# Kernel tuning notes

Hardware: AMD Instinct MI355X
Metric: run time of the kernel (lower is better)

The kernel has to match this reference:

```python
import jax, jax.numpy as jnp
import numpy as np

B, T = 512, 8192
DT = jnp.float32(1e-3)


def setup_inputs() -> dict:
    key = jax.random.key(0)
    k1, k2, k3, k4 = jax.random.split(key, 4)
    # scale noise so the 8192-step linear recurrence stays well-conditioned
    xicovs = jax.random.normal(k1, (B, T, 2, 2), jnp.float32) * 0.05
    dy = jax.random.normal(k2, (B, T, 2), jnp.float32) * 0.05
    coeffs_A = jax.random.uniform(k3, (2, 2), jnp.float32, -0.05, 0.05)  # 'uniform' init kernel
    C = jax.random.normal(k4, (2, 2), jnp.float32)
    return {"xicovs": xicovs, "dy": dy, "coeffs_A": coeffs_A, "C": C}


def reference(xicovs, dy, coeffs_A, C):
    # xicovs: [B,T,2,2], dy: [B,T,2]
    Bv = xicovs.shape[0]
    # initial state [1,0] broadcast over batch
    x0 = jnp.broadcast_to(jnp.array([1.0, 0.0], jnp.float32), (Bv, 2))
    xi_t = jnp.swapaxes(xicovs, 0, 1)  # [T,B,2,2]
    dy_t = jnp.swapaxes(dy, 0, 1)      # [T,B,2]

    def step(x, inp):
        xic, dyt = inp  # [B,2,2], [B,2]
        # cell emits C @ x_prev * dt
        out = jnp.einsum('ij,bj->bi', C, x) * DT
        A_minus_xiC = coeffs_A - jnp.einsum('bij,jk->bik', xic, C)  # [B,2,2]
        dx = jnp.einsum('bij,bj->bi', A_minus_xiC, x) * DT + jnp.einsum('bij,bj->bi', xic, dyt)
        return x + dx, out

    _, outs = jax.lax.scan(step, x0, (xi_t, dy_t))  # outs: [T,B,2]
    return jnp.swapaxes(outs, 0, 1)  # [B,T,2] (return_sequences=True)
```

## Files before the change

### kernel.cpp

```cpp
#include <hip/hip_runtime.h>


#define B_   512
#define T_   8192
#define LPT  8
#define NT   1024
static_assert(NT * LPT == T_, "one block covers one batch");

struct Aff { float m00, m01, m10, m11, v0, v1; };

__device__ __forceinline__ Aff aff_compose(const Aff& L, const Aff& E) {
    Aff r;
    r.m00 = L.m00*E.m00 + L.m01*E.m10;
    r.m01 = L.m00*E.m01 + L.m01*E.m11;
    r.m10 = L.m10*E.m00 + L.m11*E.m10;
    r.m11 = L.m10*E.m01 + L.m11*E.m11;
    r.v0  = L.m00*E.v0  + L.m01*E.v1 + L.v0;
    r.v1  = L.m10*E.v0  + L.m11*E.v1 + L.v1;
    return r;
}

__device__ __forceinline__ Aff aff_identity() {
    Aff r; r.m00 = 1.f; r.m01 = 0.f; r.m10 = 0.f; r.m11 = 1.f; r.v0 = 0.f; r.v1 = 0.f;
    return r;
}

__global__ __launch_bounds__(NT, 4) void grm_fused(
    const float* __restrict__ xic, const float* __restrict__ dy,
    const float* __restrict__ Aptr, const float* __restrict__ Cptr,
    float4* __restrict__ out4)
{
    __shared__ float4 lds4[16 * 256];

    const int b    = blockIdx.x;
    const int tid  = threadIdx.x;
    const int lane = tid & 63;
    const int wave = tid >> 6;

    float4* slice = lds4 + wave * 256;

    const float DT = 1e-3f;
    const float cd00 = Cptr[0]*DT, cd01 = Cptr[1]*DT;
    const float cd10 = Cptr[2]*DT, cd11 = Cptr[3]*DT;
    const float i00 = 1.0f + Aptr[0]*DT, i01 = Aptr[1]*DT;
    const float i10 = Aptr[2]*DT,        i11 = 1.0f + Aptr[3]*DT;

    const int wbase = b * T_ + wave * 512;
    const float4* xw = (const float4*)xic + wbase;
    const float4* dw = (const float4*)dy  + (wbase >> 1);
    float4*       ow = out4 + (wbase >> 1);

    float4 t[8], u[4];
    #pragma unroll
    for (int j = 0; j < 8; ++j) t[j] = xw[j*64 + lane];
    #pragma unroll
    for (int j = 0; j < 4; ++j) u[j] = dw[j*64 + lane];

    float4 a[LPT];
    #pragma unroll
    for (int rr = 0; rr < 2; ++rr) {
        #pragma unroll
        for (int jj = 0; jj < 4; ++jj) {
            int j = 4*rr + jj;
            int f = j*64 + lane;
            int rel = (f >> 3) & 31;
            slice[rel*8 + ((lane & 7) ^ (rel & 7))] = t[j];
        }
        if ((lane >> 5) == rr) {
            int rel = lane & 31;
            #pragma unroll
            for (int s = 0; s < LPT; ++s)
                a[s] = slice[rel*8 + (s ^ (rel & 7))];
        }
    }

    #pragma unroll
    for (int j = 0; j < 4; ++j) {
        int f = j*64 + lane;
        int o = f >> 2;
        slice[o*4 + ((lane & 3) ^ (o & 3))] = u[j];
    }
    float4 d[4];
    #pragma unroll
    for (int s = 0; s < 4; ++s)
        d[s] = slice[lane*4 + (s ^ (lane & 3))];

#define STEP_MAP(i, S)                                                  \
    {                                                                   \
        const float4 x4 = a[i];                                         \
        const float dyx = ((i)&1) ? d[(i)>>1].z : d[(i)>>1].x;          \
        const float dyy = ((i)&1) ? d[(i)>>1].w : d[(i)>>1].y;          \
        (S).m00 = i00 - (x4.x*cd00 + x4.y*cd10);                        \
        (S).m01 = i01 - (x4.x*cd01 + x4.y*cd11);                        \
        (S).m10 = i10 - (x4.z*cd00 + x4.w*cd10);                        \
        (S).m11 = i11 - (x4.z*cd01 + x4.w*cd11);                        \
        (S).v0  = x4.x*dyx + x4.y*dyy;                                  \
        (S).v1  = x4.z*dyx + x4.w*dyy;                                  \
    }

    Aff P;
    STEP_MAP(0, P);
    #pragma unroll
    for (int i = 1; i < LPT; ++i) { Aff s; STEP_MAP(i, s); P = aff_compose(s, P); }

    Aff S = P;
    #pragma unroll
    for (int sh = 1; sh < 64; sh <<= 1) {
        Aff q;
        q.m00 = __shfl_up(S.m00, sh); q.m01 = __shfl_up(S.m01, sh);
        q.m10 = __shfl_up(S.m10, sh); q.m11 = __shfl_up(S.m11, sh);
        q.v0  = __shfl_up(S.v0,  sh); q.v1  = __shfl_up(S.v1,  sh);
        if (lane >= sh) S = aff_compose(S, q);
    }

    if (lane == 63) {
        float* h = (float*)slice;
        h[0] = S.m00; h[1] = S.m01; h[2] = S.m10; h[3] = S.m11;
        h[4] = S.v0;  h[5] = S.v1;
    }
    __syncthreads();

    Aff Ew = aff_identity();
    for (int w = 0; w < wave; ++w) {
        const float* h = (const float*)(lds4 + w * 256);
        Aff t2;
        t2.m00 = h[0]; t2.m01 = h[1]; t2.m10 = h[2]; t2.m11 = h[3];
        t2.v0  = h[4]; t2.v1  = h[5];
        Ew = aff_compose(t2, Ew);
    }
    __syncthreads();

    Aff El;
    El.m00 = __shfl_up(S.m00, 1); El.m01 = __shfl_up(S.m01, 1);
    El.m10 = __shfl_up(S.m10, 1); El.m11 = __shfl_up(S.m11, 1);
    El.v0  = __shfl_up(S.v0,  1); El.v1  = __shfl_up(S.v1,  1);
    if (lane == 0) El = aff_identity();

    Aff E = aff_compose(El, Ew);
    float x0 = E.m00 + E.v0;
    float x1 = E.m10 + E.v1;

    float4 o4[4];
    #pragma unroll
    for (int i = 0; i < LPT; ++i) {
        float oxx = cd00*x0 + cd01*x1;
        float oyy = cd10*x0 + cd11*x1;
        if (i & 1) { o4[i>>1].z = oxx; o4[i>>1].w = oyy; }
        else       { o4[i>>1].x = oxx; o4[i>>1].y = oyy; }
        Aff s; STEP_MAP(i, s);
        float nx0 = s.m00*x0 + s.m01*x1 + s.v0;
        float nx1 = s.m10*x0 + s.m11*x1 + s.v1;
        x0 = nx0; x1 = nx1;
    }
#undef STEP_MAP

    #pragma unroll
    for (int s = 0; s < 4; ++s)
        slice[lane*4 + (s ^ (lane & 3))] = o4[s];
    #pragma unroll
    for (int j = 0; j < 4; ++j) {
        int f = j*64 + lane;
        int o = f >> 2;
        ow[f] = slice[o*4 + ((lane & 3) ^ (o & 3))];
    }
}

extern "C" void kernel_launch(void* const* d_in, const int* in_sizes, int n_in,
                              void* d_out, int out_size, void* d_ws, size_t ws_size,
                              hipStream_t stream) {
    const float* xic  = (const float*)d_in[0];
    const float* dy   = (const float*)d_in[1];
    const float* Aptr = (const float*)d_in[2];
    const float* Cptr = (const float*)d_in[3];
    float4* out = (float4*)d_out;

    grm_fused<<<B_, NT, 0, stream>>>(xic, dy, Aptr, Cptr, out);
}
```

Before: 140.4 us.

## Split each batch across four chained blocks with decoupled lookback state passing

Each batch row's 8192 steps are now split into four 256-thread blocks instead of one 1024-thread block. A ticket counter hands out virtual block ids in launch order, and each chunk waits on a flag for its predecessor's end state, then publishes its own through global memory. The aim is smaller blocks for better occupancy and scheduling flexibility, in exchange for a serial inter-block dependency chain, spin-waiting, and an extra memset. The LDS swizzle pattern for the dy/output transposes is also changed to reduce bank conflicts.

```diff
diff --git a/kernel.cpp b/kernel.cpp
--- a/kernel.cpp
+++ b/kernel.cpp
@@ -1,11 +1,13 @@
 #include <hip/hip_runtime.h>
 
 
-#define B_   512
-#define T_   8192
-#define LPT  8
-#define NT   1024
-static_assert(NT * LPT == T_, "one block covers one batch");
+#define B_    512
+#define T_    8192
+#define LPT   8
+#define NT    256
+#define CSTEP (NT * LPT)
+#define NCHK  (T_ / CSTEP)
+#define NBLK  (B_ * NCHK)
 
 struct Aff { float m00, m01, m10, m11, v0, v1; };
 
@@ -25,17 +27,26 @@
     return r;
 }
 
-__global__ __launch_bounds__(NT, 4) void grm_fused(
+__global__ __launch_bounds__(NT) void grm_chain(
     const float* __restrict__ xic, const float* __restrict__ dy,
     const float* __restrict__ Aptr, const float* __restrict__ Cptr,
-    float4* __restrict__ out4)
+    float4* __restrict__ out4,
+    unsigned* __restrict__ ticket, unsigned* __restrict__ flags,
+    float* __restrict__ vals)
 {
-    __shared__ float4 lds4[16 * 256];
-
-    const int b    = blockIdx.x;
+    __shared__ float4 lds4[4 * 256];
+    __shared__ float  xin_s[2];
+    __shared__ int    vid_s;
+
     const int tid  = threadIdx.x;
     const int lane = tid & 63;
     const int wave = tid >> 6;
+
+    if (tid == 0) vid_s = (int)atomicAdd(ticket, 1u);
+    __syncthreads();
+    const int vid = vid_s;
+    const int b   = vid >> 2;
+    const int c   = vid & (NCHK - 1);
 
     float4* slice = lds4 + wave * 256;
 
@@ -45,7 +56,7 @@
     const float i00 = 1.0f + Aptr[0]*DT, i01 = Aptr[1]*DT;
     const float i10 = Aptr[2]*DT,        i11 = 1.0f + Aptr[3]*DT;
 
-    const int wbase = b * T_ + wave * 512;
+    const int wbase = b * T_ + c * CSTEP + wave * 512;
     const float4* xw = (const float4*)xic + wbase;
     const float4* dw = (const float4*)dy  + (wbase >> 1);
     float4*       ow = out4 + (wbase >> 1);
@@ -78,12 +89,12 @@
     for (int j = 0; j < 4; ++j) {
         int f = j*64 + lane;
         int o = f >> 2;
-        slice[o*4 + ((lane & 3) ^ (o & 3))] = u[j];
+        slice[o*4 + ((f & 3) ^ ((o >> 1) & 3))] = u[j];
     }
     float4 d[4];
     #pragma unroll
     for (int s = 0; s < 4; ++s)
-        d[s] = slice[lane*4 + (s ^ (lane & 3))];
+        d[s] = slice[lane*4 + (s ^ ((lane >> 1) & 3))];
 
 #define STEP_MAP(i, S)                                                  \
     {                                                                   \
@@ -128,17 +139,49 @@
         t2.v0  = h[4]; t2.v1  = h[5];
         Ew = aff_compose(t2, Ew);
     }
-    __syncthreads();
+
+    if (tid == 0) {
+        Aff Tb = aff_identity();
+        #pragma unroll
+        for (int w = 0; w < 4; ++w) {
+            const float* h = (const float*)(lds4 + w * 256);
+            Aff t2;
+            t2.m00 = h[0]; t2.m01 = h[1]; t2.m10 = h[2]; t2.m11 = h[3];
+            t2.v0  = h[4]; t2.v1  = h[5];
+            Tb = aff_compose(t2, Tb);
+        }
+        float x0, x1;
+        if (c == 0) {
+            x0 = 1.0f; x1 = 0.0f;
+        } else {
+            const int p = vid - 1;
+            while (__hip_atomic_load(&flags[p], __ATOMIC_ACQUIRE,
+                                     __HIP_MEMORY_SCOPE_AGENT) == 0u)
+                __builtin_amdgcn_s_sleep(4);
+            x0 = __hip_atomic_load(&vals[2*p],   __ATOMIC_RELAXED, __HIP_MEMORY_SCOPE_AGENT);
+            x1 = __hip_atomic_load(&vals[2*p+1], __ATOMIC_RELAXED, __HIP_MEMORY_SCOPE_AGENT);
+        }
+        if (c < NCHK - 1) {
+            float y0 = Tb.m00*x0 + Tb.m01*x1 + Tb.v0;
+            float y1 = Tb.m10*x0 + Tb.m11*x1 + Tb.v1;
+            __hip_atomic_store(&vals[2*vid],   y0, __ATOMIC_RELAXED, __HIP_MEMORY_SCOPE_AGENT);
+            __hip_atomic_store(&vals[2*vid+1], y1, __ATOMIC_RELAXED, __HIP_MEMORY_SCOPE_AGENT);
+            __hip_atomic_store(&flags[vid], 1u, __ATOMIC_RELEASE, __HIP_MEMORY_SCOPE_AGENT);
+        }
+        xin_s[0] = x0; xin_s[1] = x1;
+    }
 
     Aff El;
     El.m00 = __shfl_up(S.m00, 1); El.m01 = __shfl_up(S.m01, 1);
     El.m10 = __shfl_up(S.m10, 1); El.m11 = __shfl_up(S.m11, 1);
     El.v0  = __shfl_up(S.v0,  1); El.v1  = __shfl_up(S.v1,  1);
     if (lane == 0) El = aff_identity();
-
     Aff E = aff_compose(El, Ew);
-    float x0 = E.m00 + E.v0;
-    float x1 = E.m10 + E.v1;
+
+    __syncthreads();
+    float xb0 = xin_s[0], xb1 = xin_s[1];
+    float x0 = E.m00*xb0 + E.m01*xb1 + E.v0;
+    float x1 = E.m10*xb0 + E.m11*xb1 + E.v1;
 
     float4 o4[4];
     #pragma unroll
@@ -156,12 +199,12 @@
 
     #pragma unroll
     for (int s = 0; s < 4; ++s)
-        slice[lane*4 + (s ^ (lane & 3))] = o4[s];
+        slice[lane*4 + (s ^ ((lane >> 1) & 3))] = o4[s];
     #pragma unroll
     for (int j = 0; j < 4; ++j) {
         int f = j*64 + lane;
         int o = f >> 2;
-        ow[f] = slice[o*4 + ((lane & 3) ^ (o & 3))];
+        ow[f] = slice[o*4 + ((f & 3) ^ ((o >> 1) & 3))];
     }
 }
 
@@ -174,5 +217,12 @@
     const float* Cptr = (const float*)d_in[3];
     float4* out = (float4*)d_out;
 
-    grm_fused<<<B_, NT, 0, stream>>>(xic, dy, Aptr, Cptr, out);
-}
+    char* ws = (char*)d_ws;
+    unsigned* ticket = (unsigned*)ws;
+    unsigned* flags  = (unsigned*)(ws + 256);
+    float*    vals   = (float*)(ws + 16384);
+
+    hipMemsetAsync(ws, 0, 256 + NBLK * sizeof(unsigned), stream);
+    grm_chain<<<NBLK, NT, 0, stream>>>(xic, dy, Aptr, Cptr, out,
+                                       ticket, flags, vals);
+}
```

New measurement: 255.8 us. +82.2%, slower.
